# Optimization experiments

Measured on AMD Instinct MI355X. Metric: run time of the kernel, lower is better.

Reference implementation:

```python
import jax, jax.numpy as jnp
import numpy as np


def setup_inputs() -> dict:
    key = jax.random.key(0)
    kq, kk, kv = jax.random.split(key, 3)
    B, S, D = 32, 2048, 64  # (batch*heads, seq_len, head_dim)
    q = jax.random.normal(kq, (B, S, D), dtype=jnp.float32)
    k = jax.random.normal(kk, (B, S, D), dtype=jnp.float32)
    v = jax.random.normal(kv, (B, S, D), dtype=jnp.float32)
    return {"q": q, "k": k, "v": v}


def reference(q, k, v):
    # attention = q @ k^T  (no scale, no mask: defaults scale=None, attn_mask=None)
    scores = jnp.einsum("bqd,bkd->bqk", q, k)  # [B, S, S] materialized, as in source
    attn = jax.nn.softmax(scores, axis=2)      # Softmax(dim=2) == key axis for 3D
    # dropout is identity in eval / deterministic reference
    return jnp.einsum("bqk,bkd->bqd", attn, v)
```

## Files before the change

kernel.cpp:

```cpp
#include <hip/hip_runtime.h>
#include <stdint.h>

typedef __attribute__((ext_vector_type(4)))  float    f32x4;
typedef __attribute__((ext_vector_type(16))) float    f32x16;
typedef __attribute__((ext_vector_type(8)))  _Float16 f16x8;
typedef __attribute__((ext_vector_type(8)))  __bf16   bf16x8;
typedef __attribute__((ext_vector_type(4)))  __bf16   bf16x4;
typedef __attribute__((ext_vector_type(2)))  __bf16   bf16x2;

#define SEQ   2048
#define DH    64
#define BQ    128
#define BK    64
#define NT    (SEQ / BK)
#define ROWE  72
#define TILEE (64 * ROWE)
#define L2E   1.44269504088896340736f

#if __has_builtin(__builtin_amdgcn_exp2f)
static __device__ __forceinline__ float fast_exp2(float x) { return __builtin_amdgcn_exp2f(x); }
#else
static __device__ __forceinline__ float fast_exp2(float x) {
  float r; asm("v_exp_f32 %0, %1" : "=v"(r) : "v"(x)); return r;
}
#endif

typedef const __attribute__((address_space(1))) uint32_t* gp1_t;
typedef __attribute__((address_space(3))) uint32_t*       lp3_t;


__global__ __launch_bounds__(256)
void prepass(const float* __restrict__ K, const float* __restrict__ V,
             _Float16* __restrict__ Kh, __bf16* __restrict__ Vh) {
  const int blk = blockIdx.x;
  const int tid = threadIdx.x;
  if (blk < 32 * NT) {
    const float* src = K + ((size_t)(blk >> 5) * SEQ + (size_t)(blk & 31) * 64) * DH;
    _Float16*    dst = Kh + (size_t)blk * TILEE;
    const int row = tid >> 2, c = (tid & 3) << 4;
    const float* sp = src + row * DH + c;
    f32x4 x0 = *(const f32x4*)(sp + 0),  x1 = *(const f32x4*)(sp + 4);
    f32x4 x2 = *(const f32x4*)(sp + 8),  x3 = *(const f32x4*)(sp + 12);
    f16x8 h0, h1;
#pragma unroll
    for (int j = 0; j < 4; ++j) {
      h0[j] = (_Float16)x0[j]; h0[j + 4] = (_Float16)x1[j];
      h1[j] = (_Float16)x2[j]; h1[j + 4] = (_Float16)x3[j];
    }
    *(f16x8*)(dst + row * ROWE + c)     = h0;
    *(f16x8*)(dst + row * ROWE + c + 8) = h1;
  } else {
    const int blk2 = blk - 32 * NT;
    const float* src = V + ((size_t)(blk2 >> 5) * SEQ + (size_t)(blk2 & 31) * 64) * DH;
    __bf16*      dst = Vh + (size_t)blk2 * TILEE;
#pragma unroll
    for (int it = 0; it < 4; ++it) {
      int task = tid + it * 256;
      int d = task & 63, g = task >> 6;
      const int k0i = 2 * g, k1i = 2 * g + 32, k2i = 2 * g + 1, k3i = 2 * g + 33;
      bf16x4 hv;
      hv[0] = (__bf16)src[(size_t)k0i * DH + d];
      hv[1] = (__bf16)src[(size_t)k1i * DH + d];
      hv[2] = (__bf16)src[(size_t)k2i * DH + d];
      hv[3] = (__bf16)src[(size_t)k3i * DH + d];
      *(bf16x4*)(dst + d * ROWE + 4 * g) = hv;
    }
  }
}

__global__ __launch_bounds__(256, 2)
void flash_attn_v4(const float* __restrict__ Q, const _Float16* __restrict__ Kh,
                   const __bf16* __restrict__ Vh, float* __restrict__ O) {
  __shared__ _Float16 Ksb[2][64][ROWE];
  __shared__ __bf16   Vtb[2][64][ROWE];
  __shared__ __bf16   Ps[BQ][ROWE];

  const int tid  = threadIdx.x;
  const int wv   = tid >> 6;
  const int lane = tid & 63;
  const int hfw  = lane >> 5;
  const int l31  = lane & 31;

  const int batch = blockIdx.x & 31;
  const int qblk  = blockIdx.x >> 5;

  const float* Qb = Q + (size_t)batch * SEQ * DH;
  float*       Ob = O + (size_t)batch * SEQ * DH;
  const uint32_t* Kt0 = (const uint32_t*)(Kh + (size_t)batch * NT * TILEE);
  const uint32_t* Vt0 = (const uint32_t*)(Vh + (size_t)batch * NT * TILEE);

  auto stage = [&](int t, int buf) {
    const uint32_t* kg = Kt0 + (size_t)t * (TILEE / 2);
    const uint32_t* vg = Vt0 + (size_t)t * (TILEE / 2);
    lp3_t kl = (lp3_t)&Ksb[buf][0][0];
    lp3_t vl = (lp3_t)&Vtb[buf][0][0];
#pragma unroll
    for (int j = wv; j < 9; j += 4) {
      __builtin_amdgcn_global_load_lds((gp1_t)(kg + j * 256 + lane * 4), kl + j * 256, 16, 0, 0);
      __builtin_amdgcn_global_load_lds((gp1_t)(vg + j * 256 + lane * 4), vl + j * 256, 16, 0, 0);
    }
  };

  const int qrow = qblk * BQ + wv * 32 + l31;
  f16x8 qf[4];
  {
    const float* qp = Qb + (size_t)qrow * DH + hfw * 8;
#pragma unroll
    for (int ks = 0; ks < 4; ++ks) {
      f32x4 a = *(const f32x4*)(qp + ks * 16);
      f32x4 b = *(const f32x4*)(qp + ks * 16 + 4);
#pragma unroll
      for (int j = 0; j < 4; ++j) {
        qf[ks][j]     = (_Float16)(a[j] * L2E);
        qf[ks][j + 4] = (_Float16)(b[j] * L2E);
      }
    }
  }

  f32x16 acc0 = {}, acc1 = {};
  float lsum[16];
#pragma unroll
  for (int j = 0; j < 16; ++j) lsum[j] = 0.f;

  stage(0, 0);

  for (int t = 0; t < NT; ++t) {
    __syncthreads();
    if (t + 1 < NT) stage(t + 1, (t + 1) & 1);
    const int buf = t & 1;

    f32x16 s0 = {}, s1 = {};
#pragma unroll
    for (int ks = 0; ks < 4; ++ks) {
      int dof = ks * 16 + hfw * 8;
      f16x8 kf0 = *(const f16x8*)&Ksb[buf][l31][dof];
      f16x8 kf1 = *(const f16x8*)&Ksb[buf][l31 + 32][dof];
      s0 = __builtin_amdgcn_mfma_f32_32x32x16_f16(qf[ks], kf0, s0, 0, 0, 0);
      s1 = __builtin_amdgcn_mfma_f32_32x32x16_f16(qf[ks], kf1, s1, 0, 0, 0);
    }

#pragma unroll
    for (int j = 0; j < 16; ++j) {
      float p0 = fast_exp2(s0[j]);
      float p1 = fast_exp2(s1[j]);
      lsum[j] += p0 + p1;
      int row = (j & 3) + 8 * (j >> 2) + 4 * hfw;
      bf16x2 pk; pk[0] = (__bf16)p0; pk[1] = (__bf16)p1;
      *(bf16x2*)&Ps[wv * 32 + row][2 * l31] = pk;
    }

#pragma unroll
    for (int ks = 0; ks < 4; ++ks) {
      int kof = ks * 16 + hfw * 8;
      bf16x8 pf = *(const bf16x8*)&Ps[wv * 32 + l31][kof];
      bf16x8 v0 = *(const bf16x8*)&Vtb[buf][l31][kof];
      bf16x8 v1 = *(const bf16x8*)&Vtb[buf][l31 + 32][kof];
      acc0 = __builtin_amdgcn_mfma_f32_32x32x16_bf16(pf, v0, acc0, 0, 0, 0);
      acc1 = __builtin_amdgcn_mfma_f32_32x32x16_bf16(pf, v1, acc1, 0, 0, 0);
    }
  }

#pragma unroll
  for (int j = 0; j < 16; ++j) {
    float l = lsum[j];
    l += __shfl_xor(l, 1);
    l += __shfl_xor(l, 2);
    l += __shfl_xor(l, 4);
    l += __shfl_xor(l, 8);
    l += __shfl_xor(l, 16);
    float inv = 1.0f / l;
    int row = (j & 3) + 8 * (j >> 2) + 4 * hfw;
    size_t off = (size_t)(qblk * BQ + wv * 32 + row) * DH + l31;
    Ob[off]      = acc0[j] * inv;
    Ob[off + 32] = acc1[j] * inv;
  }
}

extern "C" void kernel_launch(void* const* d_in, const int* in_sizes, int n_in,
                              void* d_out, int out_size, void* d_ws, size_t ws_size,
                              hipStream_t stream) {
  (void)in_sizes; (void)n_in; (void)ws_size; (void)out_size;
  const float* q = (const float*)d_in[0];
  const float* k = (const float*)d_in[1];
  const float* v = (const float*)d_in[2];
  float* o = (float*)d_out;
  _Float16* Kh = (_Float16*)d_ws;
  __bf16*   Vh = (__bf16*)((char*)d_ws + (size_t)32 * NT * TILEE * sizeof(_Float16));

  prepass<<<dim3(2 * 32 * NT), dim3(256), 0, stream>>>(k, v, Kh, Vh);
  flash_attn_v4<<<dim3(32 * (SEQ / BQ)), dim3(256), 0, stream>>>(q, Kh, Vh, o);
}
```

Before: 139.9 us.

## Split key loop across two wave groups per block with LDS reduction

Doubles the block to 512 threads, with two groups of four waves each handling half of the key tiles for the same 128 query rows. Partial output accumulators and row sums are combined through a shared LDS arena at the end. This raises the number of waves per CU to hide latency, but removes the double-buffered prefetch, so each tile load is now synchronously waited on before compute. It also adds an extra reduction pass through shared memory.

Result: slower. 144.9 us (+3.6%).

```diff
diff --git a/kernel.cpp b/kernel.cpp
--- a/kernel.cpp
+++ b/kernel.cpp
@@ -13,6 +13,7 @@
 #define BQ    128
 #define BK    64
 #define NT    (SEQ / BK)
+#define HT    (NT / 2)
 #define ROWE  72
 #define TILEE (64 * ROWE)
 #define L2E   1.44269504088896340736f
@@ -68,15 +69,20 @@
   }
 }
 
-__global__ __launch_bounds__(256, 2)
-void flash_attn_v4(const float* __restrict__ Q, const _Float16* __restrict__ Kh,
+__global__ __launch_bounds__(512, 4)
+void flash_attn_v5(const float* __restrict__ Q, const _Float16* __restrict__ Kh,
                    const __bf16* __restrict__ Vh, float* __restrict__ O) {
-  __shared__ _Float16 Ksb[2][64][ROWE];
-  __shared__ __bf16   Vtb[2][64][ROWE];
-  __shared__ __bf16   Ps[BQ][ROWE];
+  __shared__ __align__(16) unsigned char arena[73728];
+  _Float16 (*Ks)[64][ROWE] = (_Float16(*)[64][ROWE])(arena);
+  __bf16   (*Vt)[64][ROWE] = (__bf16(*)[64][ROWE])(arena + 18432);
+  __bf16   (*Ps)[BQ][ROWE] = (__bf16(*)[BQ][ROWE])(arena + 36864);
+  float* accAr  = (float*)arena;
+  float* lsumAr = (float*)(arena + 36864);
 
   const int tid  = threadIdx.x;
   const int wv   = tid >> 6;
+  const int wq   = wv & 3;
+  const int kg   = wv >> 2;
   const int lane = tid & 63;
   const int hfw  = lane >> 5;
   const int l31  = lane & 31;
@@ -89,19 +95,19 @@
   const uint32_t* Kt0 = (const uint32_t*)(Kh + (size_t)batch * NT * TILEE);
   const uint32_t* Vt0 = (const uint32_t*)(Vh + (size_t)batch * NT * TILEE);
 
-  auto stage = [&](int t, int buf) {
-    const uint32_t* kg = Kt0 + (size_t)t * (TILEE / 2);
-    const uint32_t* vg = Vt0 + (size_t)t * (TILEE / 2);
-    lp3_t kl = (lp3_t)&Ksb[buf][0][0];
-    lp3_t vl = (lp3_t)&Vtb[buf][0][0];
-#pragma unroll
-    for (int j = wv; j < 9; j += 4) {
-      __builtin_amdgcn_global_load_lds((gp1_t)(kg + j * 256 + lane * 4), kl + j * 256, 16, 0, 0);
-      __builtin_amdgcn_global_load_lds((gp1_t)(vg + j * 256 + lane * 4), vl + j * 256, 16, 0, 0);
+  auto stage = [&](int t) {
+    const uint32_t* kgp = Kt0 + (size_t)t * (TILEE / 2);
+    const uint32_t* vgp = Vt0 + (size_t)t * (TILEE / 2);
+    lp3_t kl = (lp3_t)&Ks[kg][0][0];
+    lp3_t vl = (lp3_t)&Vt[kg][0][0];
+#pragma unroll
+    for (int j = wq; j < 9; j += 4) {
+      __builtin_amdgcn_global_load_lds((gp1_t)(kgp + j * 256 + lane * 4), kl + j * 256, 16, 0, 0);
+      __builtin_amdgcn_global_load_lds((gp1_t)(vgp + j * 256 + lane * 4), vl + j * 256, 16, 0, 0);
     }
   };
 
-  const int qrow = qblk * BQ + wv * 32 + l31;
+  const int qrow = qblk * BQ + wq * 32 + l31;
   f16x8 qf[4];
   {
     const float* qp = Qb + (size_t)qrow * DH + hfw * 8;
@@ -122,19 +128,18 @@
 #pragma unroll
   for (int j = 0; j < 16; ++j) lsum[j] = 0.f;
 
-  stage(0, 0);
-
-  for (int t = 0; t < NT; ++t) {
+  for (int i = 0; i < HT; ++i) {
+    const int t = kg * HT + i;
     __syncthreads();
-    if (t + 1 < NT) stage(t + 1, (t + 1) & 1);
-    const int buf = t & 1;
+    stage(t);
+    __syncthreads();
 
     f32x16 s0 = {}, s1 = {};
 #pragma unroll
     for (int ks = 0; ks < 4; ++ks) {
       int dof = ks * 16 + hfw * 8;
-      f16x8 kf0 = *(const f16x8*)&Ksb[buf][l31][dof];
-      f16x8 kf1 = *(const f16x8*)&Ksb[buf][l31 + 32][dof];
+      f16x8 kf0 = *(const f16x8*)&Ks[kg][l31][dof];
+      f16x8 kf1 = *(const f16x8*)&Ks[kg][l31 + 32][dof];
       s0 = __builtin_amdgcn_mfma_f32_32x32x16_f16(qf[ks], kf0, s0, 0, 0, 0);
       s1 = __builtin_amdgcn_mfma_f32_32x32x16_f16(qf[ks], kf1, s1, 0, 0, 0);
     }
@@ -146,33 +151,67 @@
       lsum[j] += p0 + p1;
       int row = (j & 3) + 8 * (j >> 2) + 4 * hfw;
       bf16x2 pk; pk[0] = (__bf16)p0; pk[1] = (__bf16)p1;
-      *(bf16x2*)&Ps[wv * 32 + row][2 * l31] = pk;
+      *(bf16x2*)&Ps[kg][wq * 32 + row][2 * l31] = pk;
     }
 
 #pragma unroll
     for (int ks = 0; ks < 4; ++ks) {
       int kof = ks * 16 + hfw * 8;
-      bf16x8 pf = *(const bf16x8*)&Ps[wv * 32 + l31][kof];
-      bf16x8 v0 = *(const bf16x8*)&Vtb[buf][l31][kof];
-      bf16x8 v1 = *(const bf16x8*)&Vtb[buf][l31 + 32][kof];
+      bf16x8 pf = *(const bf16x8*)&Ps[kg][wq * 32 + l31][kof];
+      bf16x8 v0 = *(const bf16x8*)&Vt[kg][l31][kof];
+      bf16x8 v1 = *(const bf16x8*)&Vt[kg][l31 + 32][kof];
       acc0 = __builtin_amdgcn_mfma_f32_32x32x16_bf16(pf, v0, acc0, 0, 0, 0);
       acc1 = __builtin_amdgcn_mfma_f32_32x32x16_bf16(pf, v1, acc1, 0, 0, 0);
     }
   }
 
-#pragma unroll
-  for (int j = 0; j < 16; ++j) {
-    float l = lsum[j];
-    l += __shfl_xor(l, 1);
-    l += __shfl_xor(l, 2);
-    l += __shfl_xor(l, 4);
-    l += __shfl_xor(l, 8);
-    l += __shfl_xor(l, 16);
-    float inv = 1.0f / l;
-    int row = (j & 3) + 8 * (j >> 2) + 4 * hfw;
-    size_t off = (size_t)(qblk * BQ + wv * 32 + row) * DH + l31;
-    Ob[off]      = acc0[j] * inv;
-    Ob[off + 32] = acc1[j] * inv;
+  __syncthreads();
+  if (kg == 1) {
+    float* pa = accAr + ((wq * 64 + lane) * 36);
+#pragma unroll
+    for (int c = 0; c < 4; ++c) {
+      f32x4 t0 = { acc0[4 * c], acc0[4 * c + 1], acc0[4 * c + 2], acc0[4 * c + 3] };
+      f32x4 t1 = { acc1[4 * c], acc1[4 * c + 1], acc1[4 * c + 2], acc1[4 * c + 3] };
+      *(f32x4*)(pa + 4 * c)      = t0;
+      *(f32x4*)(pa + 16 + 4 * c) = t1;
+    }
+    float* pl = lsumAr + ((wq * 64 + lane) * 18);
+#pragma unroll
+    for (int c = 0; c < 4; ++c) {
+      f32x4 tl = { lsum[4 * c], lsum[4 * c + 1], lsum[4 * c + 2], lsum[4 * c + 3] };
+      *(f32x4*)(pl + 4 * c) = tl;
+    }
+  }
+  __syncthreads();
+  if (kg == 0) {
+    const float* pa = accAr + ((wq * 64 + lane) * 36);
+    const float* pl = lsumAr + ((wq * 64 + lane) * 18);
+#pragma unroll
+    for (int c = 0; c < 4; ++c) {
+      f32x4 t0 = *(const f32x4*)(pa + 4 * c);
+      f32x4 t1 = *(const f32x4*)(pa + 16 + 4 * c);
+      f32x4 tl = *(const f32x4*)(pl + 4 * c);
+#pragma unroll
+      for (int j = 0; j < 4; ++j) {
+        acc0[4 * c + j] += t0[j];
+        acc1[4 * c + j] += t1[j];
+        lsum[4 * c + j] += tl[j];
+      }
+    }
+#pragma unroll
+    for (int j = 0; j < 16; ++j) {
+      float l = lsum[j];
+      l += __shfl_xor(l, 1);
+      l += __shfl_xor(l, 2);
+      l += __shfl_xor(l, 4);
+      l += __shfl_xor(l, 8);
+      l += __shfl_xor(l, 16);
+      float inv = 1.0f / l;
+      int row = (j & 3) + 8 * (j >> 2) + 4 * hfw;
+      size_t off = (size_t)(qblk * BQ + wq * 32 + row) * DH + l31;
+      Ob[off]      = acc0[j] * inv;
+      Ob[off + 32] = acc1[j] * inv;
+    }
   }
 }
 
@@ -188,5 +227,5 @@
   __bf16*   Vh = (__bf16*)((char*)d_ws + (size_t)32 * NT * TILEE * sizeof(_Float16));
 
   prepass<<<dim3(2 * 32 * NT), dim3(256), 0, stream>>>(k, v, Kh, Vh);
-  flash_attn_v4<<<dim3(32 * (SEQ / BQ)), dim3(256), 0, stream>>>(q, Kh, Vh, o);
-}
+  flash_attn_v5<<<dim3(32 * (SEQ / BQ)), dim3(512), 0, stream>>>(q, Kh, Vh, o);
+}
```

## Split keys across two blocks, keep P in registers, add combine pass

Applied to the files above, without the earlier changes.

The attention kernel now splits the key range in half across two blocks per query tile (split-K), doubling grid parallelism. Partial outputs are written as bf16 along with row sums, and a new combine kernel adds and normalizes them. The QK^T MFMA operands are swapped so the exp'd scores come out in the layout needed as the PV A-fragment, with K rows permuted in the prepass. This lets P stay in registers and removes the LDS round trip and its memory. The costs are an extra kernel launch, extra global traffic for the partials, and bf16 rounding of the partial outputs.

New measurement: 147.6 us. 5.5% more time.

```diff
diff --git a/kernel.cpp b/kernel.cpp
--- a/kernel.cpp
+++ b/kernel.cpp
@@ -5,14 +5,13 @@
 typedef __attribute__((ext_vector_type(16))) float    f32x16;
 typedef __attribute__((ext_vector_type(8)))  _Float16 f16x8;
 typedef __attribute__((ext_vector_type(8)))  __bf16   bf16x8;
-typedef __attribute__((ext_vector_type(4)))  __bf16   bf16x4;
-typedef __attribute__((ext_vector_type(2)))  __bf16   bf16x2;
 
 #define SEQ   2048
 #define DH    64
 #define BQ    128
 #define BK    64
 #define NT    (SEQ / BK)
+#define HT    (NT / 2)
 #define ROWE  72
 #define TILEE (64 * ROWE)
 #define L2E   1.44269504088896340736f
@@ -24,10 +23,20 @@
   float r; asm("v_exp_f32 %0, %1" : "=v"(r) : "v"(x)); return r;
 }
 #endif
+static __device__ __forceinline__ uint32_t pack2_bf16(float a, float b) {
+  union { __bf16 h[2]; uint32_t u; } cv;
+  cv.h[0] = (__bf16)a; cv.h[1] = (__bf16)b;
+  return cv.u;
+}
+union frag_u { uint32_t u[4]; bf16x8 v; };
 
 typedef const __attribute__((address_space(1))) uint32_t* gp1_t;
 typedef __attribute__((address_space(3))) uint32_t*       lp3_t;
 
+__host__ __device__ inline int sigma32(int m) {
+  int b = m & 3, h = (m >> 2) & 1, c = m >> 3;
+  return ((c & 1) << 4) | (h << 3) | ((c >> 1) << 2) | b;
+}
 
 __global__ __launch_bounds__(256)
 void prepass(const float* __restrict__ K, const float* __restrict__ V,
@@ -38,7 +47,8 @@
     const float* src = K + ((size_t)(blk >> 5) * SEQ + (size_t)(blk & 31) * 64) * DH;
     _Float16*    dst = Kh + (size_t)blk * TILEE;
     const int row = tid >> 2, c = (tid & 3) << 4;
-    const float* sp = src + row * DH + c;
+    const int srow = (row & 32) | sigma32(row & 31);
+    const float* sp = src + srow * DH + c;
     f32x4 x0 = *(const f32x4*)(sp + 0),  x1 = *(const f32x4*)(sp + 4);
     f32x4 x2 = *(const f32x4*)(sp + 8),  x3 = *(const f32x4*)(sp + 12);
     f16x8 h0, h1;
@@ -57,23 +67,21 @@
     for (int it = 0; it < 4; ++it) {
       int task = tid + it * 256;
       int d = task & 63, g = task >> 6;
-      const int k0i = 2 * g, k1i = 2 * g + 32, k2i = 2 * g + 1, k3i = 2 * g + 33;
-      bf16x4 hv;
-      hv[0] = (__bf16)src[(size_t)k0i * DH + d];
-      hv[1] = (__bf16)src[(size_t)k1i * DH + d];
-      hv[2] = (__bf16)src[(size_t)k2i * DH + d];
-      hv[3] = (__bf16)src[(size_t)k3i * DH + d];
-      *(bf16x4*)(dst + d * ROWE + 4 * g) = hv;
-    }
-  }
-}
-
-__global__ __launch_bounds__(256, 2)
-void flash_attn_v4(const float* __restrict__ Q, const _Float16* __restrict__ Kh,
-                   const __bf16* __restrict__ Vh, float* __restrict__ O) {
+      const float* sp = src + (size_t)(4 * g) * DH + d;
+      __bf16 hv[4];
+#pragma unroll
+      for (int j = 0; j < 4; ++j) hv[j] = (__bf16)sp[(size_t)j * DH];
+      *(uint64_t*)(dst + d * ROWE + 4 * g) = *(uint64_t*)hv;
+    }
+  }
+}
+
+__global__ __launch_bounds__(256, 4)
+void flash_attn_v6(const float* __restrict__ Q, const _Float16* __restrict__ Kh,
+                   const __bf16* __restrict__ Vh, __bf16* __restrict__ Opart,
+                   float* __restrict__ lpart) {
   __shared__ _Float16 Ksb[2][64][ROWE];
   __shared__ __bf16   Vtb[2][64][ROWE];
-  __shared__ __bf16   Ps[BQ][ROWE];
 
   const int tid  = threadIdx.x;
   const int wv   = tid >> 6;
@@ -82,22 +90,23 @@
   const int l31  = lane & 31;
 
   const int batch = blockIdx.x & 31;
-  const int qblk  = blockIdx.x >> 5;
+  const int rest  = blockIdx.x >> 5;
+  const int qblk  = rest & 15;
+  const int kg    = rest >> 4;
 
   const float* Qb = Q + (size_t)batch * SEQ * DH;
-  float*       Ob = O + (size_t)batch * SEQ * DH;
   const uint32_t* Kt0 = (const uint32_t*)(Kh + (size_t)batch * NT * TILEE);
   const uint32_t* Vt0 = (const uint32_t*)(Vh + (size_t)batch * NT * TILEE);
 
   auto stage = [&](int t, int buf) {
-    const uint32_t* kg = Kt0 + (size_t)t * (TILEE / 2);
-    const uint32_t* vg = Vt0 + (size_t)t * (TILEE / 2);
+    const uint32_t* kgp = Kt0 + (size_t)t * (TILEE / 2);
+    const uint32_t* vgp = Vt0 + (size_t)t * (TILEE / 2);
     lp3_t kl = (lp3_t)&Ksb[buf][0][0];
     lp3_t vl = (lp3_t)&Vtb[buf][0][0];
 #pragma unroll
     for (int j = wv; j < 9; j += 4) {
-      __builtin_amdgcn_global_load_lds((gp1_t)(kg + j * 256 + lane * 4), kl + j * 256, 16, 0, 0);
-      __builtin_amdgcn_global_load_lds((gp1_t)(vg + j * 256 + lane * 4), vl + j * 256, 16, 0, 0);
+      __builtin_amdgcn_global_load_lds((gp1_t)(kgp + j * 256 + lane * 4), kl + j * 256, 16, 0, 0);
+      __builtin_amdgcn_global_load_lds((gp1_t)(vgp + j * 256 + lane * 4), vl + j * 256, 16, 0, 0);
     }
   };
 
@@ -118,16 +127,14 @@
   }
 
   f32x16 acc0 = {}, acc1 = {};
-  float lsum[16];
-#pragma unroll
-  for (int j = 0; j < 16; ++j) lsum[j] = 0.f;
-
-  stage(0, 0);
-
-  for (int t = 0; t < NT; ++t) {
+  float lsum = 0.f;
+
+  stage(kg * HT, 0);
+
+  for (int i = 0; i < HT; ++i) {
     __syncthreads();
-    if (t + 1 < NT) stage(t + 1, (t + 1) & 1);
-    const int buf = t & 1;
+    if (i + 1 < HT) stage(kg * HT + i + 1, (i + 1) & 1);
+    const int buf = i & 1;
 
     f32x16 s0 = {}, s1 = {};
 #pragma unroll
@@ -135,45 +142,72 @@
       int dof = ks * 16 + hfw * 8;
       f16x8 kf0 = *(const f16x8*)&Ksb[buf][l31][dof];
       f16x8 kf1 = *(const f16x8*)&Ksb[buf][l31 + 32][dof];
-      s0 = __builtin_amdgcn_mfma_f32_32x32x16_f16(qf[ks], kf0, s0, 0, 0, 0);
-      s1 = __builtin_amdgcn_mfma_f32_32x32x16_f16(qf[ks], kf1, s1, 0, 0, 0);
-    }
-
-#pragma unroll
-    for (int j = 0; j < 16; ++j) {
-      float p0 = fast_exp2(s0[j]);
-      float p1 = fast_exp2(s1[j]);
-      lsum[j] += p0 + p1;
-      int row = (j & 3) + 8 * (j >> 2) + 4 * hfw;
-      bf16x2 pk; pk[0] = (__bf16)p0; pk[1] = (__bf16)p1;
-      *(bf16x2*)&Ps[wv * 32 + row][2 * l31] = pk;
+      s0 = __builtin_amdgcn_mfma_f32_32x32x16_f16(kf0, qf[ks], s0, 0, 0, 0);
+      s1 = __builtin_amdgcn_mfma_f32_32x32x16_f16(kf1, qf[ks], s1, 0, 0, 0);
+    }
+
+    frag_u fr[4];
+#pragma unroll
+    for (int t2 = 0; t2 < 2; ++t2) {
+      const f32x16& s = t2 ? s1 : s0;
+      float p[16];
+#pragma unroll
+      for (int j = 0; j < 16; ++j) p[j] = fast_exp2(s[j]);
+      float a0 = (p[0] + p[1]) + (p[2] + p[3]);
+      float a1 = (p[4] + p[5]) + (p[6] + p[7]);
+      float a2 = (p[8] + p[9]) + (p[10] + p[11]);
+      float a3 = (p[12] + p[13]) + (p[14] + p[15]);
+      lsum += (a0 + a1) + (a2 + a3);
+      fr[2 * t2    ].u[0] = pack2_bf16(p[0],  p[1]);
+      fr[2 * t2    ].u[1] = pack2_bf16(p[2],  p[3]);
+      fr[2 * t2    ].u[2] = pack2_bf16(p[8],  p[9]);
+      fr[2 * t2    ].u[3] = pack2_bf16(p[10], p[11]);
+      fr[2 * t2 + 1].u[0] = pack2_bf16(p[4],  p[5]);
+      fr[2 * t2 + 1].u[1] = pack2_bf16(p[6],  p[7]);
+      fr[2 * t2 + 1].u[2] = pack2_bf16(p[12], p[13]);
+      fr[2 * t2 + 1].u[3] = pack2_bf16(p[14], p[15]);
     }
 
 #pragma unroll
     for (int ks = 0; ks < 4; ++ks) {
       int kof = ks * 16 + hfw * 8;
-      bf16x8 pf = *(const bf16x8*)&Ps[wv * 32 + l31][kof];
       bf16x8 v0 = *(const bf16x8*)&Vtb[buf][l31][kof];
       bf16x8 v1 = *(const bf16x8*)&Vtb[buf][l31 + 32][kof];
-      acc0 = __builtin_amdgcn_mfma_f32_32x32x16_bf16(pf, v0, acc0, 0, 0, 0);
-      acc1 = __builtin_amdgcn_mfma_f32_32x32x16_bf16(pf, v1, acc1, 0, 0, 0);
-    }
-  }
-
+      acc0 = __builtin_amdgcn_mfma_f32_32x32x16_bf16(fr[ks].v, v0, acc0, 0, 0, 0);
+      acc1 = __builtin_amdgcn_mfma_f32_32x32x16_bf16(fr[ks].v, v1, acc1, 0, 0, 0);
+    }
+  }
+
+  float tot = lsum + __shfl_xor(lsum, 32);
+  const size_t qg = (size_t)batch * SEQ + qblk * BQ;
+  lpart[(size_t)kg * 32 * SEQ + qg + wv * 32 + l31] = tot;
+  __bf16* op = Opart + (size_t)kg * 32 * SEQ * DH;
 #pragma unroll
   for (int j = 0; j < 16; ++j) {
-    float l = lsum[j];
-    l += __shfl_xor(l, 1);
-    l += __shfl_xor(l, 2);
-    l += __shfl_xor(l, 4);
-    l += __shfl_xor(l, 8);
-    l += __shfl_xor(l, 16);
-    float inv = 1.0f / l;
     int row = (j & 3) + 8 * (j >> 2) + 4 * hfw;
-    size_t off = (size_t)(qblk * BQ + wv * 32 + row) * DH + l31;
-    Ob[off]      = acc0[j] * inv;
-    Ob[off + 32] = acc1[j] * inv;
-  }
+    size_t off = (qg + wv * 32 + row) * DH + l31;
+    op[off]      = (__bf16)acc0[j];
+    op[off + 32] = (__bf16)acc1[j];
+  }
+}
+
+__global__ __launch_bounds__(256)
+void combine(const __bf16* __restrict__ Opart, const float* __restrict__ lpart,
+             float* __restrict__ O) {
+  const size_t gid  = (size_t)blockIdx.x * 256 + threadIdx.x;
+  const size_t base = gid * 8;
+  const size_t qidx = base >> 6;
+  bf16x8 a0 = *(const bf16x8*)(Opart + base);
+  bf16x8 a1 = *(const bf16x8*)(Opart + (size_t)32 * SEQ * DH + base);
+  float inv = 1.0f / (lpart[qidx] + lpart[(size_t)32 * SEQ + qidx]);
+  f32x4 o0, o1;
+#pragma unroll
+  for (int j = 0; j < 4; ++j) {
+    o0[j] = ((float)a0[j] + (float)a1[j]) * inv;
+    o1[j] = ((float)a0[j + 4] + (float)a1[j + 4]) * inv;
+  }
+  *(f32x4*)(O + base)     = o0;
+  *(f32x4*)(O + base + 4) = o1;
 }
 
 extern "C" void kernel_launch(void* const* d_in, const int* in_sizes, int n_in,
@@ -184,9 +218,13 @@
   const float* k = (const float*)d_in[1];
   const float* v = (const float*)d_in[2];
   float* o = (float*)d_out;
-  _Float16* Kh = (_Float16*)d_ws;
-  __bf16*   Vh = (__bf16*)((char*)d_ws + (size_t)32 * NT * TILEE * sizeof(_Float16));
+  char* w = (char*)d_ws;
+  _Float16* Kh    = (_Float16*)w;                    w += (size_t)32 * NT * TILEE * 2;
+  __bf16*   Vh    = (__bf16*)w;                      w += (size_t)32 * NT * TILEE * 2;
+  __bf16*   Opart = (__bf16*)w;                      w += (size_t)2 * 32 * SEQ * DH * 2;
+  float*    lpart = (float*)w;
 
   prepass<<<dim3(2 * 32 * NT), dim3(256), 0, stream>>>(k, v, Kh, Vh);
-  flash_attn_v4<<<dim3(32 * (SEQ / BQ)), dim3(256), 0, stream>>>(q, Kh, Vh, o);
-}
+  flash_attn_v6<<<dim3(32 * 16 * 2), dim3(256), 0, stream>>>(q, Kh, Vh, Opart, lpart);
+  combine<<<dim3((32 * SEQ * DH) / (256 * 8)), dim3(256), 0, stream>>>(Opart, lpart, o);
+}
```
